# Optimization experiments

Measured on AMD Instinct MI355X. Metric: run time of the kernel, lower is better.

The kernel has to match this reference:

```python
import jax, jax.numpy as jnp
import numpy as np

N_NODES = 100000
N_EDGES = 3200000
D = 128
BN_EPS = 1e-5


def setup_inputs() -> dict:
    key = jax.random.key(0)
    k1, k2, k3, k4 = jax.random.split(key, 4)
    x = jax.random.normal(k1, (N_NODES, D), dtype=jnp.float32)
    edge_index = jax.random.randint(k2, (2, N_EDGES), 0, N_NODES, dtype=jnp.int64)
    # GCNConv linear weight, torch nn.Linear convention: [out_dim, in_dim]
    W = jax.random.normal(k3, (D, D), dtype=jnp.float32) * (1.0 / np.sqrt(D))
    # BatchNorm1d affine params
    gamma = jnp.ones((D,), dtype=jnp.float32) + 0.1 * jax.random.normal(k4, (D,), dtype=jnp.float32)
    beta = jnp.zeros((D,), dtype=jnp.float32)
    return {"x": x, "edge_index": edge_index, "W": W, "gamma": gamma, "beta": beta}


def reference(x, edge_index, W, gamma, beta):
    # GCNConv(bias=False, add_self_loops=False), then BN (batch stats), ReLU, skip-add.
    src, dst = edge_index[0], edge_index[1]
    n = x.shape[0]

    # linear transform: [N, D_out]
    h = x @ W.T

    # symmetric GCN normalization: deg over destination, norm = d^-1/2[src]*d^-1/2[dst]
    ones = jnp.ones((src.shape[0],), dtype=x.dtype)
    deg = jax.ops.segment_sum(ones, dst, num_segments=n)
    dinv = jnp.where(deg > 0, jax.lax.rsqrt(jnp.maximum(deg, 1.0)), 0.0)
    norm = dinv[src] * dinv[dst]  # [E]

    # gather-message-scatter: [E, D] -> [N, D]
    msg = h[src] * norm[:, None]
    agg = jax.ops.segment_sum(msg, dst, num_segments=n)

    # BatchNorm1d in training mode (batch statistics, biased variance)
    mean = jnp.mean(agg, axis=0)
    var = jnp.mean(jnp.square(agg - mean), axis=0)
    bn = (agg - mean) * jax.lax.rsqrt(var + BN_EPS) * gamma + beta

    # ReLU + residual skip (dims match)
    out = jax.nn.relu(bn) + x
    return out
```

## Files before the change

### kernel.cpp

```cpp
#include <hip/hip_runtime.h>
#include <hip/hip_bf16.h>
#include <cstdint>
#include <cstddef>

#define D 128
#define SBLK 512
#define SBBITS 10
#define NSB 128
#define TILE 4096
#define BINT 512

typedef __attribute__((ext_vector_type(8))) short short8;
typedef __attribute__((ext_vector_type(4))) float f32x4;

__device__ __forceinline__ unsigned short f2bf(float f) {
    union { float f; unsigned u; } v; v.f = f;
    unsigned r = v.u + 0x7FFF + ((v.u >> 16) & 1);
    return (unsigned short)(r >> 16);
}
__device__ __forceinline__ float bflo(unsigned p) {
    union { unsigned u; float f; } v; v.u = p << 16; return v.f;
}
__device__ __forceinline__ float bfhi(unsigned p) {
    union { unsigned u; float f; } v; v.u = p & 0xFFFF0000u; return v.f;
}
__device__ __forceinline__ float bf2f(unsigned short u) {
    union { unsigned u; float f; } v; v.u = ((unsigned)u) << 16; return v.f;
}

__global__ __launch_bounds__(256) void k_prep(const unsigned* __restrict__ ei, int E,
                                              int* __restrict__ flag,
                                              const float* __restrict__ W,
                                              unsigned short* __restrict__ Wbf,
                                              int* __restrict__ g_sbcnt) {
    int t = threadIdx.x, b = blockIdx.x;
    int i = b * 256 + t;
    if (i < D * D) Wbf[i] = f2bf(W[i]);
    if (b == 0 && t == 0) {
        int n = E < 256 ? E : 256;
        int allz = 1;
        for (int k = 0; k < n; ++k) {
            if (ei[2 * k + 1] != 0u) { allz = 0; break; }
        }
        *flag = allz;
    }
    if (b == 63 && t < NSB) g_sbcnt[t] = 0;
}

__global__ __launch_bounds__(256) void k_gemm(const float* __restrict__ x,
                                              const unsigned short* __restrict__ Wbf,
                                              unsigned short* __restrict__ h, int M) {
    __shared__ unsigned short sx[64 * 136];
    int t = threadIdx.x;
    int base = blockIdx.x * 64;

#pragma unroll
    for (int j = 0; j < 8; ++j) {
        int idx = j * 256 + t;
        int row = idx >> 5, c4 = (idx & 31) * 4;
        int gr = base + row;
        float4 v = (gr < M) ? *(const float4*)(x + (size_t)gr * D + c4)
                            : make_float4(0.f, 0.f, 0.f, 0.f);
        unsigned short* dst = &sx[row * 136 + c4];
        dst[0] = f2bf(v.x); dst[1] = f2bf(v.y); dst[2] = f2bf(v.z); dst[3] = f2bf(v.w);
    }
    __syncthreads();

    int wave = t >> 6, lane = t & 63;
    int lr = lane & 15, lg = lane >> 4;
    int lrow = wave * 16 + lr;
    f32x4 acc[8];
#pragma unroll
    for (int i = 0; i < 8; ++i) acc[i] = (f32x4){0.f, 0.f, 0.f, 0.f};

#pragma unroll
    for (int ks = 0; ks < 4; ++ks) {
        int k0 = ks * 32 + lg * 8;
        short8 af = *(const short8*)(&sx[lrow * 136 + k0]);
#pragma unroll
        for (int nt = 0; nt < 8; ++nt) {
            short8 bf = *(const short8*)(Wbf + (size_t)(nt * 16 + lr) * D + k0);
            acc[nt] = __builtin_amdgcn_mfma_f32_16x16x32_bf16(af, bf, acc[nt], 0, 0, 0);
        }
    }
    int m0 = base + wave * 16;
#pragma unroll
    for (int nt = 0; nt < 8; ++nt) {
#pragma unroll
        for (int r = 0; r < 4; ++r) {
            int rr = m0 + lg * 4 + r;
            if (rr < M) h[(size_t)rr * D + nt * 16 + lr] = f2bf(acc[nt][r]);
        }
    }
}

__global__ __launch_bounds__(BINT) void k_bin(const int* __restrict__ ei, int E,
                                              const int* __restrict__ flagp,
                                              int* __restrict__ g_sbcnt,
                                              unsigned* __restrict__ binned, int C2) {
    __shared__ unsigned stage[TILE];
    __shared__ unsigned char ssb[TILE];
    __shared__ int hcnt[NSB], hoff[NSB], lcur[NSB], gbase[NSB];
    int f64 = *flagp;
    int t = threadIdx.x;
    int base = blockIdx.x * TILE;
    int cnt = E - base; if (cnt > TILE) cnt = TILE;

    if (t < NSB) hcnt[t] = 0;
    __syncthreads();

    unsigned ent[8]; int esb[8];
#pragma unroll
    for (int j = 0; j < 8; ++j) {
        int idx = j * BINT + t;
        esb[j] = -1;
        if (idx < cnt) {
            int e = base + idx;
            int s, d;
            if (f64) {
                s = ((const int2*)ei)[e].x;
                d = ((const int2*)ei)[E + e].x;
            } else {
                s = ei[e];
                d = ei[E + e];
            }
            esb[j] = d >> SBBITS;
            ent[j] = (unsigned)s | ((unsigned)(d & ((1 << SBBITS) - 1)) << 17);
            atomicAdd(&hcnt[esb[j]], 1);
        }
    }
    __syncthreads();
    if (t < NSB) hoff[t] = hcnt[t];
    __syncthreads();
#pragma unroll
    for (int off = 1; off < NSB; off <<= 1) {
        int a = (t < NSB && t >= off) ? hoff[t - off] : 0;
        __syncthreads();
        if (t < NSB) hoff[t] += a;
        __syncthreads();
    }
    if (t < NSB) {
        int ex = hoff[t] - hcnt[t];
        lcur[t] = ex;
        hoff[t] = ex;
        gbase[t] = (hcnt[t] > 0) ? atomicAdd(&g_sbcnt[t], hcnt[t]) : 0;
    }
    __syncthreads();
#pragma unroll
    for (int j = 0; j < 8; ++j) {
        if (esb[j] >= 0) {
            int p = atomicAdd(&lcur[esb[j]], 1);
            stage[p] = ent[j];
            ssb[p] = (unsigned char)esb[j];
        }
    }
    __syncthreads();
    for (int i = t; i < cnt; i += BINT) {
        int sb = ssb[i];
        int pos = gbase[sb] + (i - hoff[sb]);
        if (pos < C2) binned[(size_t)sb * C2 + pos] = stage[i];
    }
}

__global__ __launch_bounds__(1024) void k_fill2(const unsigned* __restrict__ binned, int C2,
                                                const int* __restrict__ g_sbcnt,
                                                int2* __restrict__ ronode,
                                                float* __restrict__ dinv,
                                                int* __restrict__ csrc, int N) {
    __shared__ int deg[1024];
    __shared__ int scn[1024];
    __shared__ int cur[1024];
    int b = blockIdx.x, t = threadIdx.x;
    int cnt = g_sbcnt[b]; if (cnt > C2) cnt = C2;
    const unsigned* ent = binned + (size_t)b * C2;

    deg[t] = 0;
    __syncthreads();
    for (int i = t; i < cnt; i += 1024) atomicAdd(&deg[ent[i] >> 17], 1);
    __syncthreads();
    scn[t] = deg[t];
    __syncthreads();
    for (int off = 1; off < 1024; off <<= 1) {
        int a = (t >= off) ? scn[t - off] : 0;
        __syncthreads();
        scn[t] += a;
        __syncthreads();
    }
    int ex = scn[t] - deg[t];
    cur[t] = ex;
    int node = (b << SBBITS) + t;
    if (node < N) {
        ronode[node] = make_int2(b * C2 + ex, deg[t]);
        dinv[node] = deg[t] > 0 ? rsqrtf((float)deg[t]) : 0.0f;
    }
    __syncthreads();
    for (int i = t; i < cnt; i += 1024) {
        unsigned e = ent[i];
        int pos = atomicAdd(&cur[e >> 17], 1);
        csrc[b * C2 + pos] = (int)(e & 0x1FFFF);
    }
}

__global__ __launch_bounds__(256) void k_agg(const unsigned long long* __restrict__ h,
                                             const int* __restrict__ csrc,
                                             const int2* __restrict__ ronode,
                                             const float* __restrict__ dinv,
                                             ushort4* __restrict__ aggb, int N) {
    int wave = threadIdx.x >> 6, lane = threadIdx.x & 63;
    int node = blockIdx.x * 4 + wave;
    if (node >= N) return;
    int half = lane >> 5, lq = lane & 31;
    int2 ro = ronode[node];
    int beg = ro.x, end = ro.x + ro.y;
    float a0 = 0.f, a1 = 0.f, a2 = 0.f, a3 = 0.f;
    int i = beg;
    for (; i + 16 <= end; i += 16) {
#pragma unroll
        for (int p = 0; p < 8; ++p) {
            int e = i + 2 * p + half;
            int s = csrc[e];
            float w = dinv[s];
            unsigned long long pk = h[(size_t)s * 32 + lq];
            unsigned lo = (unsigned)pk, hi = (unsigned)(pk >> 32);
            a0 += w * bflo(lo); a1 += w * bfhi(lo);
            a2 += w * bflo(hi); a3 += w * bfhi(hi);
        }
    }
    for (; i + 2 <= end; i += 2) {
        int e = i + half;
        int s = csrc[e];
        float w = dinv[s];
        unsigned long long pk = h[(size_t)s * 32 + lq];
        unsigned lo = (unsigned)pk, hi = (unsigned)(pk >> 32);
        a0 += w * bflo(lo); a1 += w * bfhi(lo);
        a2 += w * bflo(hi); a3 += w * bfhi(hi);
    }
    if (i < end) {
        int s = csrc[i];
        float w = half ? 0.f : dinv[s];
        unsigned long long pk = h[(size_t)s * 32 + lq];
        unsigned lo = (unsigned)pk, hi = (unsigned)(pk >> 32);
        a0 += w * bflo(lo); a1 += w * bfhi(lo);
        a2 += w * bflo(hi); a3 += w * bfhi(hi);
    }
    a0 += __shfl_xor(a0, 32);
    a1 += __shfl_xor(a1, 32);
    a2 += __shfl_xor(a2, 32);
    a3 += __shfl_xor(a3, 32);
    float sd = dinv[node];
    if (half == 0) {
        ushort4 o;
        o.x = f2bf(a0 * sd); o.y = f2bf(a1 * sd);
        o.z = f2bf(a2 * sd); o.w = f2bf(a3 * sd);
        aggb[(size_t)node * 32 + lq] = o;
    }
}

__global__ __launch_bounds__(256) void k_stats(const unsigned short* __restrict__ aggb,
                                               float* __restrict__ part, int N) {
    int t = threadIdx.x;
    int c = t & 127, half = t >> 7;
    float s = 0.f, q = 0.f;
    for (int r = blockIdx.x * 2 + half; r < N; r += SBLK * 2) {
        float v = bf2f(aggb[(size_t)r * 128 + c]);
        s += v; q += v * v;
    }
    __shared__ float sh[512];
    sh[t] = s; sh[256 + t] = q;
    __syncthreads();
    if (t < 128) {
        part[blockIdx.x * 256 + t]       = sh[t] + sh[t + 128];
        part[blockIdx.x * 256 + 128 + t] = sh[256 + t] + sh[256 + t + 128];
    }
}

__global__ void k_params(const float* __restrict__ part, const float* __restrict__ gamma,
                         const float* __restrict__ beta, float* __restrict__ params, int N) {
    int t = threadIdx.x;
    float a = 0.f;
    for (int b = 0; b < SBLK; ++b) a += part[b * 256 + t];
    __shared__ float sh[256];
    sh[t] = a;
    __syncthreads();
    if (t < 128) {
        float mean = sh[t] / (float)N;
        float var = sh[128 + t] / (float)N - mean * mean;
        var = var > 0.f ? var : 0.f;
        float sc = gamma[t] * rsqrtf(var + 1e-5f);
        params[t] = sc;
        params[128 + t] = beta[t] - mean * sc;
    }
}

__global__ __launch_bounds__(256) void k_final(float4* __restrict__ out,
                                               const ushort4* __restrict__ aggb,
                                               const float4* __restrict__ x,
                                               const float* __restrict__ params, int n4) {
    const float4* p4 = (const float4*)params;
    for (int i = blockIdx.x * 256 + threadIdx.x; i < n4; i += gridDim.x * 256) {
        int c = i & 31;
        float4 s = p4[c], b = p4[32 + c];
        ushort4 av = aggb[i];
        float4 xv = x[i];
        float4 r;
        r.x = fmaxf(bf2f(av.x) * s.x + b.x, 0.f) + xv.x;
        r.y = fmaxf(bf2f(av.y) * s.y + b.y, 0.f) + xv.y;
        r.z = fmaxf(bf2f(av.z) * s.z + b.z, 0.f) + xv.z;
        r.w = fmaxf(bf2f(av.w) * s.w + b.w, 0.f) + xv.w;
        out[i] = r;
    }
}

extern "C" void kernel_launch(void* const* d_in, const int* in_sizes, int n_in,
                              void* d_out, int out_size, void* d_ws, size_t ws_size,
                              hipStream_t stream) {
    const float* x     = (const float*)d_in[0];
    const int*   ei    = (const int*)d_in[1];
    const float* W     = (const float*)d_in[2];
    const float* gamma = (const float*)d_in[3];
    const float* beta  = (const float*)d_in[4];

    int N = in_sizes[0] / D;
    int E = in_sizes[1] / 2;
    int NSBu = (N + (1 << SBBITS) - 1) >> SBBITS;
    int avg = (E + NSBu - 1) / NSBu;
    int C2 = ((avg + 4096 + 63) / 64) * 64;

    char* ws = (char*)d_ws;
    size_t off = 0;
    auto alloc = [&](size_t bytes) { size_t o = off; off = (off + bytes + 255) & ~(size_t)255; return o; };

    size_t binned_bytes = (size_t)NSBu * C2 * 4;
    size_t aggb_bytes   = (size_t)N * D * 2;
    size_t share_bytes  = binned_bytes > aggb_bytes ? binned_bytes : aggb_bytes;

    unsigned short* h    = (unsigned short*)(ws + alloc((size_t)N * D * 2));
    int*      csrc   = (int*)     (ws + alloc((size_t)NSBu * C2 * 4));
    char*     share  =            (ws + alloc(share_bytes));
    unsigned* binned = (unsigned*)share;
    unsigned short* aggb = (unsigned short*)share;
    int*      g_sbcnt= (int*)     (ws + alloc((size_t)NSB * 4));
    float*    dinv   = (float*)   (ws + alloc((size_t)N * 4));
    int2*     ronode = (int2*)    (ws + alloc((size_t)N * 8));
    float*    part   = (float*)   (ws + alloc((size_t)SBLK * 256 * 4));
    float*    params = (float*)   (ws + alloc(256 * 4));
    int*      flagp  = (int*)     (ws + alloc(4));
    unsigned short* Wbf = (unsigned short*)(ws + alloc((size_t)D * D * 2));

    k_prep<<<64, 256, 0, stream>>>((const unsigned*)ei, E, flagp, W, Wbf, g_sbcnt);
    k_gemm<<<(N + 63) / 64, 256, 0, stream>>>(x, Wbf, h, N);
    k_bin<<<(E + TILE - 1) / TILE, BINT, 0, stream>>>(ei, E, flagp, g_sbcnt, binned, C2);
    k_fill2<<<NSBu, 1024, 0, stream>>>(binned, C2, g_sbcnt, ronode, dinv, csrc, N);
    k_agg<<<(N + 3) / 4, 256, 0, stream>>>((const unsigned long long*)h, csrc, ronode, dinv,
                                           (ushort4*)aggb, N);
    k_stats<<<SBLK, 256, 0, stream>>>(aggb, part, N);
    k_params<<<1, 256, 0, stream>>>(part, gamma, beta, params, N);
    k_final<<<2048, 256, 0, stream>>>((float4*)d_out, (const ushort4*)aggb,
                                      (const float4*)x, params, (N * D) / 4);
}
```

Before: 376.5 us.

## Stage GEMM output through LDS, halve superblock size, vectorize BN stats

The GEMM epilogue now writes bf16 results into shared memory and then stores whole rows to global memory with 16-byte stores, replacing scattered 2-byte writes. Destination superblocks shrink from 1024 to 512 nodes, which doubles the number of bins and fill blocks so CSR construction gets more parallelism. The stats kernel reads four bf16 values per load with eight row groups per block and fewer blocks. Together these cut uncoalesced store traffic and give the fill stage more concurrency. The cost is extra syncthreads in the GEMM, and half the threads sit idle during the scan in fill2.

```diff
diff --git a/kernel.cpp b/kernel.cpp
--- a/kernel.cpp
+++ b/kernel.cpp
@@ -4,9 +4,10 @@
 #include <cstddef>
 
 #define D 128
-#define SBLK 512
-#define SBBITS 10
-#define NSB 128
+#define SBLK 256
+#define SBBITS 9
+#define SBN 512
+#define NSB 256
 #define TILE 4096
 #define BINT 512
 
@@ -44,7 +45,7 @@
         }
         *flag = allz;
     }
-    if (b == 63 && t < NSB) g_sbcnt[t] = 0;
+    if (b == 63) g_sbcnt[t] = 0;
 }
 
 __global__ __launch_bounds__(256) void k_gemm(const float* __restrict__ x,
@@ -83,13 +84,23 @@
             acc[nt] = __builtin_amdgcn_mfma_f32_16x16x32_bf16(af, bf, acc[nt], 0, 0, 0);
         }
     }
-    int m0 = base + wave * 16;
+    __syncthreads();
 #pragma unroll
     for (int nt = 0; nt < 8; ++nt) {
 #pragma unroll
         for (int r = 0; r < 4; ++r) {
-            int rr = m0 + lg * 4 + r;
-            if (rr < M) h[(size_t)rr * D + nt * 16 + lr] = f2bf(acc[nt][r]);
+            sx[(wave * 16 + lg * 4 + r) * 136 + nt * 16 + lr] = f2bf(acc[nt][r]);
+        }
+    }
+    __syncthreads();
+#pragma unroll
+    for (int j = 0; j < 4; ++j) {
+        int idx = j * 256 + t;
+        int row = idx >> 4, c8 = (idx & 15) * 8;
+        int gr = base + row;
+        if (gr < M) {
+            short8 v = *(const short8*)(&sx[row * 136 + c8]);
+            *(short8*)(h + (size_t)gr * D + c8) = v;
         }
     }
 }
@@ -125,7 +136,7 @@
                 d = ei[E + e];
             }
             esb[j] = d >> SBBITS;
-            ent[j] = (unsigned)s | ((unsigned)(d & ((1 << SBBITS) - 1)) << 17);
+            ent[j] = (unsigned)s | ((unsigned)(d & (SBN - 1)) << 17);
             atomicAdd(&hcnt[esb[j]], 1);
         }
     }
@@ -167,31 +178,33 @@
                                                 int2* __restrict__ ronode,
                                                 float* __restrict__ dinv,
                                                 int* __restrict__ csrc, int N) {
-    __shared__ int deg[1024];
-    __shared__ int scn[1024];
-    __shared__ int cur[1024];
+    __shared__ int deg[SBN];
+    __shared__ int scn[SBN];
+    __shared__ int cur[SBN];
     int b = blockIdx.x, t = threadIdx.x;
     int cnt = g_sbcnt[b]; if (cnt > C2) cnt = C2;
     const unsigned* ent = binned + (size_t)b * C2;
 
-    deg[t] = 0;
+    if (t < SBN) deg[t] = 0;
     __syncthreads();
     for (int i = t; i < cnt; i += 1024) atomicAdd(&deg[ent[i] >> 17], 1);
     __syncthreads();
-    scn[t] = deg[t];
-    __syncthreads();
-    for (int off = 1; off < 1024; off <<= 1) {
-        int a = (t >= off) ? scn[t - off] : 0;
+    if (t < SBN) scn[t] = deg[t];
+    __syncthreads();
+    for (int off = 1; off < SBN; off <<= 1) {
+        int a = (t < SBN && t >= off) ? scn[t - off] : 0;
         __syncthreads();
-        scn[t] += a;
+        if (t < SBN) scn[t] += a;
         __syncthreads();
     }
-    int ex = scn[t] - deg[t];
-    cur[t] = ex;
-    int node = (b << SBBITS) + t;
-    if (node < N) {
-        ronode[node] = make_int2(b * C2 + ex, deg[t]);
-        dinv[node] = deg[t] > 0 ? rsqrtf((float)deg[t]) : 0.0f;
+    if (t < SBN) {
+        int ex = scn[t] - deg[t];
+        cur[t] = ex;
+        int node = (b << SBBITS) + t;
+        if (node < N) {
+            ronode[node] = make_int2(b * C2 + ex, deg[t]);
+            dinv[node] = deg[t] > 0 ? rsqrtf((float)deg[t]) : 0.0f;
+        }
     }
     __syncthreads();
     for (int i = t; i < cnt; i += 1024) {
@@ -256,21 +269,32 @@
     }
 }
 
-__global__ __launch_bounds__(256) void k_stats(const unsigned short* __restrict__ aggb,
+__global__ __launch_bounds__(256) void k_stats(const ushort4* __restrict__ aggb,
                                                float* __restrict__ part, int N) {
     int t = threadIdx.x;
-    int c = t & 127, half = t >> 7;
-    float s = 0.f, q = 0.f;
-    for (int r = blockIdx.x * 2 + half; r < N; r += SBLK * 2) {
-        float v = bf2f(aggb[(size_t)r * 128 + c]);
-        s += v; q += v * v;
-    }
-    __shared__ float sh[512];
-    sh[t] = s; sh[256 + t] = q;
-    __syncthreads();
-    if (t < 128) {
-        part[blockIdx.x * 256 + t]       = sh[t] + sh[t + 128];
-        part[blockIdx.x * 256 + 128 + t] = sh[256 + t] + sh[256 + t + 128];
+    int c4 = t & 31, rg = t >> 5;
+    float s0 = 0.f, s1 = 0.f, s2 = 0.f, s3 = 0.f;
+    float q0 = 0.f, q1 = 0.f, q2 = 0.f, q3 = 0.f;
+    for (int r = blockIdx.x * 8 + rg; r < N; r += SBLK * 8) {
+        ushort4 u = aggb[(size_t)r * 32 + c4];
+        float v0 = bf2f(u.x), v1 = bf2f(u.y), v2 = bf2f(u.z), v3 = bf2f(u.w);
+        s0 += v0; s1 += v1; s2 += v2; s3 += v3;
+        q0 += v0 * v0; q1 += v1 * v1; q2 += v2 * v2; q3 += v3 * v3;
+    }
+    __shared__ float4 shs[256], shq[256];
+    shs[t] = make_float4(s0, s1, s2, s3);
+    shq[t] = make_float4(q0, q1, q2, q3);
+    __syncthreads();
+    if (t < 32) {
+        float4 as = shs[t], aq = shq[t];
+#pragma unroll
+        for (int k = 1; k < 8; ++k) {
+            float4 bs = shs[t + 32 * k], bq = shq[t + 32 * k];
+            as.x += bs.x; as.y += bs.y; as.z += bs.z; as.w += bs.w;
+            aq.x += bq.x; aq.y += bq.y; aq.z += bq.z; aq.w += bq.w;
+        }
+        *(float4*)&part[blockIdx.x * 256 + t * 4]       = as;
+        *(float4*)&part[blockIdx.x * 256 + 128 + t * 4] = aq;
     }
 }
 
@@ -322,7 +346,7 @@
 
     int N = in_sizes[0] / D;
     int E = in_sizes[1] / 2;
-    int NSBu = (N + (1 << SBBITS) - 1) >> SBBITS;
+    int NSBu = (N + SBN - 1) >> SBBITS;
     int avg = (E + NSBu - 1) / NSBu;
     int C2 = ((avg + 4096 + 63) / 64) * 64;
 
@@ -353,7 +377,7 @@
     k_fill2<<<NSBu, 1024, 0, stream>>>(binned, C2, g_sbcnt, ronode, dinv, csrc, N);
     k_agg<<<(N + 3) / 4, 256, 0, stream>>>((const unsigned long long*)h, csrc, ronode, dinv,
                                            (ushort4*)aggb, N);
-    k_stats<<<SBLK, 256, 0, stream>>>(aggb, part, N);
+    k_stats<<<SBLK, 256, 0, stream>>>((const ushort4*)aggb, part, N);
     k_params<<<1, 256, 0, stream>>>(part, gamma, beta, params, N);
     k_final<<<2048, 256, 0, stream>>>((float4*)d_out, (const ushort4*)aggb,
                                       (const float4*)x, params, (N * D) / 4);
```

Result: faster. 342.1 us (-9.2%).
